# Kernel optimization log

Measured on AMD Instinct MI355X. Metric: run time of the kernel, lower is better.

The kernel has to match this reference:

```python
import jax, jax.numpy as jnp
import numpy as np

B, N_PER, H, EMB, V, S, L = 128, 205, 200, 768, 50265, 512, 6
N = B * N_PER

def conv1d(x, w, b, pad):
    # x: [B, Cin, L], w: [Cout, Cin, K]
    out = jax.lax.conv_general_dilated(x, w, (1,), [(pad, pad)],
                                       dimension_numbers=('NCH', 'OIH', 'NCH'))
    return out + b[None, :, None]

def setup_inputs() -> dict:
    key = jax.random.key(0)
    ks = jax.random.split(key, 24)
    s = lambda fan: 1.0 / np.sqrt(fan)
    inp = {
        'x': jax.random.normal(ks[0], (N, H), jnp.float32),
        'edge_index': jax.random.randint(ks[1], (2, 209920), 0, N, jnp.int32),
        'input_ids': jax.random.randint(ks[2], (B, S), 0, V, jnp.int32),
        'embed_table': jax.random.normal(ks[3], (V, EMB), jnp.float32) * 0.02,
        'ggc_w': jax.random.normal(ks[4], (L, H, H), jnp.float32) * s(H),
        'gru_wih': jax.random.normal(ks[5], (3 * H, H), jnp.float32) * s(H),
        'gru_whh': jax.random.normal(ks[6], (3 * H, H), jnp.float32) * s(H),
        'gru_bih': jnp.zeros((3 * H,), jnp.float32),
        'gru_bhh': jnp.zeros((3 * H,), jnp.float32),
        'conv0_w': jax.random.normal(ks[7], (200, 200, 3), jnp.float32) * s(200 * 3),
        'conv0_b': jnp.zeros((200,), jnp.float32),
        'conv1_w': jax.random.normal(ks[8], (200, EMB, 3), jnp.float32) * s(EMB * 3),
        'conv1_b': jnp.zeros((200,), jnp.float32),
        'conv2_w': jax.random.normal(ks[9], (200, EMB, 4), jnp.float32) * s(EMB * 4),
        'conv2_b': jnp.zeros((200,), jnp.float32),
        'conv3_w': jax.random.normal(ks[10], (200, EMB, 5), jnp.float32) * s(EMB * 5),
        'conv3_b': jnp.zeros((200,), jnp.float32),
        'fc1_w': jax.random.normal(ks[11], (256, 800), jnp.float32) * s(800),
        'fc1_b': jnp.zeros((256,), jnp.float32),
        'fc2_w': jax.random.normal(ks[12], (128, 256), jnp.float32) * s(256),
        'fc2_b': jnp.zeros((128,), jnp.float32),
        'fc3_w': jax.random.normal(ks[13], (2, 128), jnp.float32) * s(128),
        'fc3_b': jnp.zeros((2,), jnp.float32),
    }
    return inp

def gated_graph_conv(x, edge_index, ggc_w, wih, whh, bih, bhh):
    src, dst = edge_index[0], edge_index[1]
    h = x  # [N, H], in_dim == out_channels so no padding needed
    for i in range(L):
        m = h @ ggc_w[i]                                   # [N, H]
        agg = jax.ops.segment_sum(m[src], dst, num_segments=N)  # scatter-add at targets
        gi = agg @ wih.T + bih                             # [N, 3H]
        gh = h @ whh.T + bhh
        ir, iz, inn = jnp.split(gi, 3, axis=1)
        hr, hz, hn = jnp.split(gh, 3, axis=1)
        r = jax.nn.sigmoid(ir + hr)
        z = jax.nn.sigmoid(iz + hz)
        n = jnp.tanh(inn + r * hn)
        h = (1.0 - z) * n + z * h
    return h

def reference(x, edge_index, input_ids, embed_table, ggc_w, gru_wih, gru_whh,
              gru_bih, gru_bhh, conv0_w, conv0_b, conv1_w, conv1_b, conv2_w,
              conv2_b, conv3_w, conv3_b, fc1_w, fc1_b, fc2_w, fc2_b, fc3_w, fc3_b):
    g = gated_graph_conv(x, edge_index, ggc_w, gru_wih, gru_whh, gru_bih, gru_bhh)
    g = g.reshape(B, N_PER, H).transpose(0, 2, 1)          # [B, 200, N_PER]
    e = embed_table[input_ids].transpose(0, 2, 1)          # [B, 768, S]
    x0 = jax.nn.relu(conv1d(g, conv0_w, conv0_b, 1))
    x1 = jax.nn.relu(conv1d(e, conv1_w, conv1_b, 0))
    x2 = jax.nn.relu(conv1d(e, conv2_w, conv2_b, 0))
    x3 = jax.nn.relu(conv1d(e, conv3_w, conv3_b, 0))
    feats = jnp.concatenate([x0.max(axis=2), x1.max(axis=2),
                             x2.max(axis=2), x3.max(axis=2)], axis=1)  # [B, 800]
    h = jax.nn.relu(feats @ fc1_w.T + fc1_b)   # dropout is identity in eval
    h = jax.nn.relu(h @ fc2_w.T + fc2_b)
    return h @ fc3_w.T + fc3_b                 # [B, 2]
```

## Files before the change

kernel.cpp:

```cpp
#include <hip/hip_runtime.h>
#include <math.h>

namespace {

constexpr int NB    = 128;
constexpr int NPER  = 205;
constexpr int H     = 200;
constexpr int EMBD  = 768;
constexpr int SEQ   = 512;
constexpr int NLAY  = 6;
constexpr int NNODE = NB * NPER;
constexpr int NEDGE = 209920;

typedef __bf16 bf16;
typedef _Float16 f16;
typedef __attribute__((ext_vector_type(8))) __bf16 bf16x8;
typedef __attribute__((ext_vector_type(8))) _Float16 f16x8;
typedef __attribute__((ext_vector_type(4))) float f32x4;
typedef unsigned short ushort8 __attribute__((ext_vector_type(8)));
typedef float float4v __attribute__((ext_vector_type(4)));

__device__ __forceinline__ float sigm(float x) { return 1.0f / (1.0f + expf(-x)); }

__device__ __forceinline__ unsigned short f2bf(float x) {
    unsigned int u = __float_as_uint(x);
    unsigned int r = (u + 0x7fffu + ((u >> 16) & 1u)) >> 16;
    return (unsigned short)r;
}
__device__ __forceinline__ unsigned short f2h(float x) {
    union { f16 h; unsigned short u; } c;
    c.h = (f16)x;
    return c.u;
}
__device__ __forceinline__ float h2f(unsigned short u) {
    union { unsigned short u; f16 h; } c;
    c.u = u;
    return (float)c.h;
}

__device__ __forceinline__ int pk_unit(int row, int s) {
    int q = row >> 1;
    return q * 8 + ((((row & 1) << 2) | s) ^ (q & 7));
}

template<bool BIAS, bool OUTF16>
__global__ __launch_bounds__(256, 4)
void gemm_w64(const unsigned short* __restrict__ A, int lda,
              const unsigned short* __restrict__ B,
              const float* __restrict__ bias, int Mreal, int Nreal,
              float* __restrict__ Cf, unsigned short* __restrict__ Ch,
              int ldc, int Kpad)
{
    __shared__ unsigned short As[128 * 64];
    __shared__ unsigned short Bs[128 * 64];

    const int p0 = blockIdx.x * 128;
    const int o0 = blockIdx.y * 128;
    const int tid = threadIdx.x, lane = tid & 63, wid = tid >> 6;
    const int wm = wid >> 1, wn = wid & 1;
    const int lrow = lane & 15, lk = lane >> 4;

    f32x4 acc[4][4];
    #pragma unroll
    for (int i = 0; i < 4; ++i)
        #pragma unroll
        for (int j = 0; j < 4; ++j) acc[i][j] = (f32x4){0.f, 0.f, 0.f, 0.f};

    for (int c0 = 0; c0 < Kpad; c0 += 64) {
        __syncthreads();
        for (int i = wid; i < 32; i += 4) {
            if (i < 16) {
                int u = i * 64 + lane;
                int row = u >> 3, slot = u & 7;
                int ss = slot ^ (row & 7);
                const unsigned short* sA = A + (size_t)(p0 + row) * lda + c0 + ss * 8;
                __builtin_amdgcn_global_load_lds(
                    (const __attribute__((address_space(1))) void*)sA,
                    (__attribute__((address_space(3))) void*)(As + i * 512), 16, 0, 0);
            } else {
                int i2 = i - 16;
                int u = i2 * 64 + lane;
                int row = u >> 3, slot = u & 7;
                int ss = slot ^ (row & 7);
                const unsigned short* sB = B + (size_t)(o0 + row) * Kpad + c0 + ss * 8;
                __builtin_amdgcn_global_load_lds(
                    (const __attribute__((address_space(1))) void*)sB,
                    (__attribute__((address_space(3))) void*)(Bs + i2 * 512), 16, 0, 0);
            }
        }
        __syncthreads();
        #pragma unroll
        for (int hf = 0; hf < 2; ++hf) {
            f16x8 vb[4];
            #pragma unroll
            for (int fn = 0; fn < 4; ++fn) {
                int r = wn * 64 + fn * 16 + lrow;
                int sl = (hf * 4 + lk) ^ (r & 7);
                vb[fn] = *reinterpret_cast<const f16x8*>(&Bs[r * 64 + sl * 8]);
            }
            #pragma unroll
            for (int fm = 0; fm < 4; ++fm) {
                int r = wm * 64 + fm * 16 + lrow;
                int sl = (hf * 4 + lk) ^ (r & 7);
                f16x8 va = *reinterpret_cast<const f16x8*>(&As[r * 64 + sl * 8]);
                #pragma unroll
                for (int fn = 0; fn < 4; ++fn)
                    acc[fm][fn] = __builtin_amdgcn_mfma_f32_16x16x32_f16(va, vb[fn], acc[fm][fn], 0, 0, 0);
            }
        }
    }
    #pragma unroll
    for (int fn = 0; fn < 4; ++fn) {
        int o = o0 + wn * 64 + fn * 16 + lrow;
        if (o >= Nreal) continue;
        float bv = BIAS ? bias[o] : 0.0f;
        #pragma unroll
        for (int fm = 0; fm < 4; ++fm) {
            #pragma unroll
            for (int i = 0; i < 4; ++i) {
                int p = p0 + wm * 64 + fm * 16 + lk * 4 + i;
                if (p >= Mreal) continue;
                float v = acc[fm][fn][i] + bv;
                if (OUTF16) Ch[(size_t)p * ldc + o] = f2h(v);
                else        Cf[(size_t)p * ldc + o] = v;
            }
        }
    }
}

__global__ __launch_bounds__(256, 2)
void gemm_gru(const unsigned short* __restrict__ A,
              const unsigned short* __restrict__ B,
              const float* __restrict__ bb,
              unsigned short* __restrict__ Hn)
{
    __shared__ unsigned short As[2][128 * 64];
    __shared__ unsigned short Bs[2][128 * 64];

    const int p0 = blockIdx.x * 128;
    const int o0 = blockIdx.y * 128;
    const int tid = threadIdx.x, lane = tid & 63, wid = tid >> 6;
    const int wm = wid >> 1, wn = wid & 1;
    const int lrow = lane & 15, lk = lane >> 4;

    auto stage = [&](int bs, int c0) {
        for (int i = wid; i < 32; i += 4) {
            if (i < 16) {
                int u = i * 64 + lane;
                int row = u >> 3, slot = u & 7;
                int ss = slot ^ (row & 7);
                const unsigned short* sA = A + (size_t)(p0 + row) * 512 + c0 + ss * 8;
                __builtin_amdgcn_global_load_lds(
                    (const __attribute__((address_space(1))) void*)sA,
                    (__attribute__((address_space(3))) void*)(&As[bs][i * 512]), 16, 0, 0);
            } else {
                int i2 = i - 16;
                int u = i2 * 64 + lane;
                int row = u >> 3, slot = u & 7;
                int ss = slot ^ (row & 7);
                const unsigned short* sB = B + (size_t)(o0 + row) * 512 + c0 + ss * 8;
                __builtin_amdgcn_global_load_lds(
                    (const __attribute__((address_space(1))) void*)sB,
                    (__attribute__((address_space(3))) void*)(&Bs[bs][i2 * 512]), 16, 0, 0);
            }
        }
    };

    f32x4 acc[4][4];
    #pragma unroll
    for (int i = 0; i < 4; ++i)
        #pragma unroll
        for (int j = 0; j < 4; ++j) acc[i][j] = (f32x4){0.f, 0.f, 0.f, 0.f};

    stage(0, 0);
    __syncthreads();
    int bs = 0;
    for (int t = 0; t < 8; ++t) {
        if (t + 1 < 8) stage(bs ^ 1, (t + 1) * 64);
        const unsigned short* Asc = As[bs];
        const unsigned short* Bsc = Bs[bs];
        #pragma unroll
        for (int hf = 0; hf < 2; ++hf) {
            f16x8 vb[4];
            #pragma unroll
            for (int fn = 0; fn < 4; ++fn) {
                int r = wn * 64 + fn * 16 + lrow;
                int sl = (hf * 4 + lk) ^ (r & 7);
                vb[fn] = *reinterpret_cast<const f16x8*>(&Bsc[r * 64 + sl * 8]);
            }
            #pragma unroll
            for (int fm = 0; fm < 4; ++fm) {
                int r = wm * 64 + fm * 16 + lrow;
                int sl = (hf * 4 + lk) ^ (r & 7);
                f16x8 va = *reinterpret_cast<const f16x8*>(&Asc[r * 64 + sl * 8]);
                #pragma unroll
                for (int fn = 0; fn < 4; ++fn)
                    acc[fm][fn] = __builtin_amdgcn_mfma_f32_16x16x32_f16(va, vb[fn], acc[fm][fn], 0, 0, 0);
            }
        }
        __syncthreads();
        bs ^= 1;
    }

    const int colbase = o0 + wn * 64;
    const int c = (colbase >> 2) + lrow;
    float b0 = bb[colbase + 0 * 16 + lrow];
    float b1 = bb[colbase + 1 * 16 + lrow];
    float b2 = bb[colbase + 2 * 16 + lrow];
    float b3 = bb[colbase + 3 * 16 + lrow];
    #pragma unroll
    for (int fm = 0; fm < 4; ++fm) {
        #pragma unroll
        for (int i = 0; i < 4; ++i) {
            int p = p0 + wm * 64 + fm * 16 + lk * 4 + i;
            size_t hidx = (size_t)p * 512 + 256 + c;
            if (c < H) {
                float r = sigm(acc[fm][0][i] + b0);
                float z = sigm(acc[fm][1][i] + b1);
                float nn = tanhf((acc[fm][2][i] + b2) + r * (acc[fm][3][i] + b3));
                float ho = h2f(A[hidx]);
                Hn[hidx] = f2h((1.0f - z) * nn + z * ho);
            } else {
                Hn[hidx] = 0;
            }
        }
    }
}

template<int K, int CINP, int LIN, int LOUT>
__global__ __launch_bounds__(512, 4)
void conv_w64(const unsigned short* __restrict__ E, const unsigned short* __restrict__ WT,
              const float* __restrict__ bias, int COUT,
              float* __restrict__ feats, int foff)
{
    constexpr int AROWS  = 272;
    constexpr int AINSTR = AROWS * 4 / 64;
    constexpr int BINSTR = K * 128 * 4 / 64;
    __shared__ unsigned short As[AROWS * 32];
    __shared__ unsigned short Bs[K * 128 * 32];

    const int p0 = blockIdx.x * 256;
    const int o0 = blockIdx.y * 128;
    const int b  = blockIdx.z;
    const int tid = threadIdx.x, lane = tid & 63, wid = tid >> 6;
    const int wm = wid >> 1, wn = wid & 1;
    const int lrow = lane & 15, lk = lane >> 4;

    const unsigned short* Eb = E + (size_t)b * LIN * CINP;

    f32x4 acc[4][4];
    #pragma unroll
    for (int i = 0; i < 4; ++i)
        #pragma unroll
        for (int j = 0; j < 4; ++j) acc[i][j] = (f32x4){0.f, 0.f, 0.f, 0.f};

    for (int c0 = 0; c0 < CINP; c0 += 32) {
        __syncthreads();
        for (int i = wid; i < AINSTR + BINSTR; i += 8) {
            if (i < AINSTR) {
                int u = i * 64 + lane;
                int q = u >> 3, cs = u & 7;
                int bsw = cs ^ (q & 7);
                int row = q * 2 + (bsw >> 2), s = bsw & 3;
                int srow = p0 + row; if (srow > LIN - 1) srow = LIN - 1;
                const unsigned short* src = Eb + (size_t)srow * CINP + c0 + s * 8;
                __builtin_amdgcn_global_load_lds(
                    (const __attribute__((address_space(1))) void*)src,
                    (__attribute__((address_space(3))) void*)(As + i * 512), 16, 0, 0);
            } else {
                int i2 = i - AINSTR;
                int u = i2 * 64 + lane;
                int q = u >> 3, cs = u & 7;
                int bsw = cs ^ (q & 7);
                int R = q * 2 + (bsw >> 2), s = bsw & 3;
                int k = R >> 7, r = R & 127;
                const unsigned short* src = WT + ((size_t)k * 256 + o0 + r) * CINP + c0 + s * 8;
                __builtin_amdgcn_global_load_lds(
                    (const __attribute__((address_space(1))) void*)src,
                    (__attribute__((address_space(3))) void*)(Bs + i2 * 512), 16, 0, 0);
            }
        }
        __syncthreads();
        #pragma unroll
        for (int k = 0; k < K; ++k) {
            bf16x8 vb[4];
            #pragma unroll
            for (int fn = 0; fn < 4; ++fn) {
                int R = k * 128 + wn * 64 + fn * 16 + lrow;
                vb[fn] = *reinterpret_cast<const bf16x8*>(&Bs[pk_unit(R, lk) * 8]);
            }
            #pragma unroll
            for (int fm = 0; fm < 4; ++fm) {
                int r = wm * 64 + fm * 16 + lrow + k;
                bf16x8 va = *reinterpret_cast<const bf16x8*>(&As[pk_unit(r, lk) * 8]);
                #pragma unroll
                for (int fn = 0; fn < 4; ++fn)
                    acc[fm][fn] = __builtin_amdgcn_mfma_f32_16x16x32_bf16(va, vb[fn], acc[fm][fn], 0, 0, 0);
            }
        }
    }
    #pragma unroll
    for (int fn = 0; fn < 4; ++fn) {
        int o = o0 + wn * 64 + fn * 16 + lrow;
        float mx = 0.0f;
        if (o < COUT) {
            float bv = bias[o];
            #pragma unroll
            for (int fm = 0; fm < 4; ++fm)
                #pragma unroll
                for (int i = 0; i < 4; ++i) {
                    int p = p0 + wm * 64 + fm * 16 + lk * 4 + i;
                    if (p < LOUT) mx = fmaxf(mx, acc[fm][fn][i] + bv);
                }
        }
        mx = fmaxf(mx, __shfl_xor(mx, 16));
        mx = fmaxf(mx, __shfl_xor(mx, 32));
        if (lane < 16 && o < COUT)
            atomicMax((int*)&feats[(size_t)b * 800 + foff + o], __float_as_int(mx));
    }
}

__global__ void hist_kernel(const int* __restrict__ dst, int* __restrict__ deg)
{
    int e = blockIdx.x * 256 + threadIdx.x;
    if (e < NEDGE) atomicAdd(&deg[dst[e]], 1);
}

__global__ void scan_kernel(const int* __restrict__ deg, int* __restrict__ off, int* __restrict__ cur)
{
    __shared__ int part[1024];
    const int tid = threadIdx.x;
    const int CH = (NNODE + 1023) / 1024;
    int base = tid * CH;
    int s = 0;
    for (int i = 0; i < CH; ++i) { int idx = base + i; s += (idx < NNODE ? deg[idx] : 0); }
    part[tid] = s;
    __syncthreads();
    for (int d = 1; d < 1024; d <<= 1) {
        int v = (tid >= d) ? part[tid - d] : 0;
        __syncthreads();
        part[tid] += v;
        __syncthreads();
    }
    int run = tid ? part[tid - 1] : 0;
    for (int i = 0; i < CH; ++i) {
        int idx = base + i;
        if (idx < NNODE) { off[idx] = run; cur[idx] = run; run += deg[idx]; }
    }
    if (tid == 1023) off[NNODE] = run;
}

__global__ void fill_kernel(const int* __restrict__ src, const int* __restrict__ dst,
                            int* __restrict__ cur, int* __restrict__ eidx)
{
    int e = blockIdx.x * 256 + threadIdx.x;
    if (e >= NEDGE) return;
    int d = dst[e];
    int pos = atomicAdd(&cur[d], 1);
    eidx[pos] = src[e];
}

__global__ void gather_h2(const int* __restrict__ off, const int* __restrict__ eidx,
                          unsigned short* __restrict__ acat)
{
    int t = blockIdx.x * 256 + threadIdx.x;
    if (t >= NNODE * 32) return;
    int c8 = t & 31, n = t >> 5;
    float s[8] = {0.f, 0.f, 0.f, 0.f, 0.f, 0.f, 0.f, 0.f};
    if (c8 < 25) {
        const size_t cb = (size_t)c8 * 8;
        int beg = off[n], end = off[n + 1];
        for (int i = beg; i < end; ++i) {
            int sn = eidx[i];
            ushort8 hh = *(const ushort8*)(acat + (size_t)sn * 512 + 256 + cb);
            #pragma unroll
            for (int j = 0; j < 8; ++j) s[j] += h2f(hh[j]);
        }
    }
    ushort8 o;
    #pragma unroll
    for (int j = 0; j < 8; ++j) o[j] = f2h(s[j]);
    *(ushort8*)(acat + (size_t)n * 512 + c8 * 8) = o;
}

__global__ void h0_kernel(const float* __restrict__ x, unsigned short* __restrict__ acat)
{
    int t = blockIdx.x * 256 + threadIdx.x;
    if (t >= NNODE * 32) return;
    int c8 = t & 31, n = t >> 5;
    ushort8 o = {0,0,0,0,0,0,0,0};
    if (c8 < 25) {
        const float* src = x + (size_t)n * H + c8 * 8;
        float4v v0 = *(const float4v*)src;
        float4v v1 = *(const float4v*)(src + 4);
        o[0] = f2h(v0[0]); o[1] = f2h(v0[1]); o[2] = f2h(v0[2]); o[3] = f2h(v0[3]);
        o[4] = f2h(v1[0]); o[5] = f2h(v1[1]); o[6] = f2h(v1[2]); o[7] = f2h(v1[3]);
    }
    *(ushort8*)(acat + (size_t)n * 512 + 256 + c8 * 8) = o;
}

__global__ void wih16p_prep(const float* __restrict__ wih, unsigned short* __restrict__ w16)
{
    int t = blockIdx.x * 256 + threadIdx.x;
    if (t >= 896 * 32) return;
    int c8 = t & 31, r = t >> 5;
    int g = (r >> 4) & 3;
    int c = (r >> 6) * 16 + (r & 15);
    ushort8 o = {0,0,0,0,0,0,0,0};
    if (g < 3 && c < H) {
        #pragma unroll
        for (int j = 0; j < 8; ++j) {
            int k = c8 * 8 + j;
            if (k < H) o[j] = f2h(wih[(size_t)(g * 200 + c) * H + k]);
        }
    }
    *(ushort8*)(w16 + (size_t)r * 256 + c8 * 8) = o;
}

__global__ void wl_prep(const float* __restrict__ w, unsigned short* __restrict__ wl)
{
    int t = blockIdx.x * 256 + threadIdx.x;
    if (t >= NLAY * 256 * 32) return;
    int c8 = t & 31;
    int rest = t >> 5;
    int jr = rest & 255;
    int l = rest >> 8;
    ushort8 o = {0,0,0,0,0,0,0,0};
    if (jr < H) {
        #pragma unroll
        for (int j = 0; j < 8; ++j) {
            int k = c8 * 8 + j;
            if (k < H) o[j] = f2h(w[(size_t)l * H * H + (size_t)jr * H + k]);
        }
    }
    *(ushort8*)(wl + (size_t)l * 65536 + (size_t)jr * 256 + c8 * 8) = o;
}

__global__ void wf_rightp(const float* __restrict__ whh, const float* __restrict__ bih,
                          const float* __restrict__ bhh,
                          unsigned short* __restrict__ Wf, float* __restrict__ bb)
{
    int t = blockIdx.x * 256 + threadIdx.x;
    if (t >= NLAY * 896 * 32) return;
    int c8 = t & 31;
    int rest = t >> 5;
    int r = rest % 896;
    int l = rest / 896;
    int g = (r >> 4) & 3;
    int c = (r >> 6) * 16 + (r & 15);
    ushort8 o = {0,0,0,0,0,0,0,0};
    if (c < H) {
        #pragma unroll
        for (int j = 0; j < 8; ++j) {
            int kk = c8 * 8 + j;
            float v = 0.0f;
            if (kk < H) {
                if (g == 0)      v = whh[(size_t)c * H + kk];
                else if (g == 1) v = whh[(size_t)(200 + c) * H + kk];
                else if (g == 3) v = whh[(size_t)(400 + c) * H + kk];
            }
            o[j] = f2h(v);
        }
    }
    *(ushort8*)(Wf + (size_t)l * 458752 + (size_t)r * 512 + 256 + c8 * 8) = o;
    if (l == 0 && c8 == 0) {
        float bv = 0.0f;
        if (c < H) {
            if (g == 0)      bv = bih[c] + bhh[c];
            else if (g == 1) bv = bih[200 + c] + bhh[200 + c];
            else if (g == 2) bv = bih[400 + c];
            else             bv = bhh[400 + c];
        }
        bb[r] = bv;
    }
}

__global__ void embed_bf16_kernel(const int* __restrict__ ids, const float* __restrict__ table,
                                  unsigned short* __restrict__ e)
{
    int t = blockIdx.x * 256 + threadIdx.x;
    const int total = NB * SEQ * (EMBD / 8);
    if (t >= total) return;
    int j = t % (EMBD / 8), row = t / (EMBD / 8);
    int id = ids[row];
    const float* src = table + (size_t)id * EMBD + j * 8;
    float4v v0 = *(const float4v*)src;
    float4v v1 = *(const float4v*)(src + 4);
    ushort8 o;
    o[0] = f2bf(v0[0]); o[1] = f2bf(v0[1]); o[2] = f2bf(v0[2]); o[3] = f2bf(v0[3]);
    o[4] = f2bf(v1[0]); o[5] = f2bf(v1[1]); o[6] = f2bf(v1[2]); o[7] = f2bf(v1[3]);
    *(ushort8*)(e + (size_t)row * EMBD + j * 8) = o;
}

__global__ void h_pad_from_acat(const unsigned short* __restrict__ acat,
                                unsigned short* __restrict__ e0)
{
    int t = blockIdx.x * 256 + threadIdx.x;
    const int total = NB * 208 * 32;
    if (t >= total) return;
    int c8 = t % 32, rest = t / 32;
    int r = rest % 208, b = rest / 208;
    ushort8 o = {0,0,0,0,0,0,0,0};
    if (r >= 1 && r <= 205) {
        int node = b * NPER + (r - 1);
        ushort8 hh = *(const ushort8*)(acat + (size_t)node * 512 + 256 + c8 * 8);
        #pragma unroll
        for (int j = 0; j < 8; ++j) o[j] = f2bf(h2f(hh[j]));
    }
    *(ushort8*)(e0 + ((size_t)(b * 208 + r)) * 256 + c8 * 8) = o;
}

__global__ void wconv_bf16_kernel(const float* __restrict__ w, unsigned short* __restrict__ wt,
                                  int K, int CINP, int CINR, int COUT)
{
    long long t = (long long)blockIdx.x * 256 + threadIdx.x;
    long long total = (long long)K * 256 * CINP;
    if (t >= total) return;
    int cin = (int)(t % CINP);
    long long rest = t / CINP;
    int o = (int)(rest % 256), k = (int)(rest / 256);
    float v = 0.0f;
    if (o < COUT && cin < CINR) v = w[((size_t)o * CINR + cin) * K + k];
    wt[t] = f2bf(v);
}

__global__ __launch_bounds__(256)
void fc_head(const float* __restrict__ feats,
             const float* __restrict__ w1, const float* __restrict__ b1,
             const float* __restrict__ w2, const float* __restrict__ b2,
             const float* __restrict__ w3, const float* __restrict__ b3,
             float* __restrict__ out)
{
    __shared__ float f[800];
    __shared__ float h1[256];
    __shared__ float h2[128];
    const int b = blockIdx.x, tid = threadIdx.x;
    for (int i = tid; i < 800; i += 256) f[i] = feats[(size_t)b * 800 + i];
    __syncthreads();
    {
        float acc = b1[tid];
        const float* wr = w1 + (size_t)tid * 800;
        for (int k = 0; k < 800; ++k) acc = fmaf(f[k], wr[k], acc);
        h1[tid] = fmaxf(acc, 0.0f);
    }
    __syncthreads();
    if (tid < 128) {
        float acc = b2[tid];
        const float* wr = w2 + (size_t)tid * 256;
        for (int k = 0; k < 256; ++k) acc = fmaf(h1[k], wr[k], acc);
        h2[tid] = fmaxf(acc, 0.0f);
    }
    __syncthreads();
    if (tid < 2) {
        float acc = b3[tid];
        const float* wr = w3 + (size_t)tid * 128;
        for (int k = 0; k < 128; ++k) acc = fmaf(h2[k], wr[k], acc);
        out[(size_t)b * 2 + tid] = acc;
    }
}

}

extern "C" void kernel_launch(void* const* d_in, const int* in_sizes, int n_in,
                              void* d_out, int out_size, void* d_ws, size_t ws_size,
                              hipStream_t stream)
{
    const float* x         = (const float*)d_in[0];
    const int*   edge      = (const int*)d_in[1];
    const int*   input_ids = (const int*)d_in[2];
    const float* table     = (const float*)d_in[3];
    const float* ggc_w     = (const float*)d_in[4];
    const float* wih       = (const float*)d_in[5];
    const float* whh       = (const float*)d_in[6];
    const float* bih       = (const float*)d_in[7];
    const float* bhh       = (const float*)d_in[8];
    const float* c0w = (const float*)d_in[9];  const float* c0b = (const float*)d_in[10];
    const float* c1w = (const float*)d_in[11]; const float* c1b = (const float*)d_in[12];
    const float* c2w = (const float*)d_in[13]; const float* c2b = (const float*)d_in[14];
    const float* c3w = (const float*)d_in[15]; const float* c3b = (const float*)d_in[16];
    const float* f1w = (const float*)d_in[17]; const float* f1b = (const float*)d_in[18];
    const float* f2w = (const float*)d_in[19]; const float* f2b = (const float*)d_in[20];
    const float* f3w = (const float*)d_in[21]; const float* f3b = (const float*)d_in[22];
    float* out = (float*)d_out;

    float* ws = (float*)d_ws;
    unsigned short* acat_a = (unsigned short*)(ws + 0);
    unsigned short* acat_b = (unsigned short*)(ws + 6717440);
    unsigned short* Wf     = (unsigned short*)(ws + 13434880);
    unsigned short* wl16   = (unsigned short*)(ws + 14811136);
    unsigned short* wih16p = (unsigned short*)(ws + 15007744);
    float* b_big = ws + 15122432;
    int* deg  = (int*)(ws + 15123328);
    int* off  = (int*)(ws + 15149568);
    int* cur  = (int*)(ws + 15175809);
    int* eidx = (int*)(ws + 15202050);
    unsigned short* e_bf16 = (unsigned short*)(ws + 0);
    unsigned short* e0     = (unsigned short*)(ws + 25165824);
    unsigned short* wt0    = (unsigned short*)(ws + 28600000);
    unsigned short* wt1    = wt0 + (size_t)3 * 256 * 256;
    unsigned short* wt2    = wt1 + (size_t)3 * 256 * EMBD;
    unsigned short* wt3    = wt2 + (size_t)4 * 256 * EMBD;
    float* feats = ws + 29900000;

    const int* srcp = edge;
    const int* dstp = edge + NEDGE;

    dim3 blk(256);
    dim3 blk512(512);

    hipMemsetAsync(deg, 0, sizeof(int) * NNODE, stream);
    hipMemsetAsync(acat_b, 0, (size_t)NNODE * 512 * 2, stream);
    hist_kernel<<<dim3((NEDGE + 255) / 256), blk, 0, stream>>>(dstp, deg);
    scan_kernel<<<dim3(1), dim3(1024), 0, stream>>>(deg, off, cur);
    fill_kernel<<<dim3((NEDGE + 255) / 256), blk, 0, stream>>>(srcp, dstp, cur, eidx);
    h0_kernel<<<dim3((NNODE * 32 + 255) / 256), blk, 0, stream>>>(x, acat_a);
    wih16p_prep<<<dim3((896 * 32 + 255) / 256), blk, 0, stream>>>(wih, wih16p);
    wl_prep<<<dim3((NLAY * 256 * 32 + 255) / 256), blk, 0, stream>>>(ggc_w, wl16);
    hipMemsetAsync(Wf, 0, (size_t)NLAY * 896 * 512 * 2, stream);
    wf_rightp<<<dim3((NLAY * 896 * 32 + 255) / 256), blk, 0, stream>>>(whh, bih, bhh, Wf, b_big);
    for (int l = 0; l < NLAY; ++l) {
        gemm_w64<false, true><<<dim3(7, 2), blk, 0, stream>>>(
            wih16p, 256, wl16 + (size_t)l * 65536, nullptr, 896, 200,
            nullptr, Wf + (size_t)l * 458752, 512, 256);
    }

    unsigned short* bufs[2] = { acat_a, acat_b };
    for (int l = 0; l < NLAY; ++l) {
        unsigned short* curb = bufs[l & 1];
        unsigned short* nxtb = bufs[(l + 1) & 1];
        gather_h2<<<dim3((NNODE * 32 + 255) / 256), blk, 0, stream>>>(off, eidx, curb);
        gemm_gru<<<dim3(NNODE / 128, 7), blk, 0, stream>>>(
            curb, Wf + (size_t)l * 458752, b_big, nxtb);
    }

    h_pad_from_acat<<<dim3((NB * 208 * 32 + 255) / 256), blk, 0, stream>>>(acat_a, e0);
    embed_bf16_kernel<<<dim3(NB * SEQ * (EMBD / 8) / 256), blk, 0, stream>>>(input_ids, table, e_bf16);
    wconv_bf16_kernel<<<dim3((3 * 256 * 256 + 255) / 256), blk, 0, stream>>>(c0w, wt0, 3, 256, 200, 200);
    wconv_bf16_kernel<<<dim3((3 * 256 * EMBD + 255) / 256), blk, 0, stream>>>(c1w, wt1, 3, EMBD, EMBD, 200);
    wconv_bf16_kernel<<<dim3((4 * 256 * EMBD + 255) / 256), blk, 0, stream>>>(c2w, wt2, 4, EMBD, EMBD, 200);
    wconv_bf16_kernel<<<dim3((5 * 256 * EMBD + 255) / 256), blk, 0, stream>>>(c3w, wt3, 5, EMBD, EMBD, 200);

    hipMemsetAsync(feats, 0, sizeof(float) * NB * 800, stream);
    conv_w64<3, 256, 208, 205><<<dim3(1, 2, NB), blk512, 0, stream>>>(e0, wt0, c0b, 200, feats, 0);
    conv_w64<3, EMBD, SEQ, 510><<<dim3(2, 2, NB), blk512, 0, stream>>>(e_bf16, wt1, c1b, 200, feats, 200);
    conv_w64<4, EMBD, SEQ, 509><<<dim3(2, 2, NB), blk512, 0, stream>>>(e_bf16, wt2, c2b, 200, feats, 400);
    conv_w64<5, EMBD, SEQ, 508><<<dim3(2, 2, NB), blk512, 0, stream>>>(e_bf16, wt3, c3b, 200, feats, 600);

    fc_head<<<dim3(NB), blk, 0, stream>>>(feats, f1w, f1b, f2w, f2b, f3w, f3b, out);
}
```

Measured before the change: 1.040 ms.

## Shrink concatenated GRU operand row stride from 512 to 448 and batch weight GEMMs

Repacks the concatenated [aggregated | hidden] fp16 operand and fused GRU weight rows from a 512 stride to 448, with the hidden half at offset 224. The GRU GEMM then runs 7 K-iterations instead of 8, which cuts MFMA work and memory traffic per layer. The per-layer weight-fusion GEMMs are merged into one launch using blockIdx.z, and the memset of the second activation buffer is removed, since the padding columns are no longer written. The gather kernel is unrolled by four edges to get more loads in flight. The risk is that stale padding in the alternate buffer must stay harmless: padding columns 200-223 in acat_b are never zeroed, so their contents depend on the matching weight columns being zero.

```diff
diff --git a/kernel.cpp b/kernel.cpp
--- a/kernel.cpp
+++ b/kernel.cpp
@@ -11,6 +11,8 @@
 constexpr int NLAY  = 6;
 constexpr int NNODE = NB * NPER;
 constexpr int NEDGE = 209920;
+constexpr int KP    = 448;
+constexpr int HOFF  = 224;
 
 typedef __bf16 bf16;
 typedef _Float16 f16;
@@ -46,9 +48,9 @@
 template<bool BIAS, bool OUTF16>
 __global__ __launch_bounds__(256, 4)
 void gemm_w64(const unsigned short* __restrict__ A, int lda,
-              const unsigned short* __restrict__ B,
+              const unsigned short* __restrict__ B, size_t strideBz,
               const float* __restrict__ bias, int Mreal, int Nreal,
-              float* __restrict__ Cf, unsigned short* __restrict__ Ch,
+              float* __restrict__ Cf, unsigned short* __restrict__ Ch, size_t strideCz,
               int ldc, int Kpad)
 {
     __shared__ unsigned short As[128 * 64];
@@ -56,6 +58,7 @@
 
     const int p0 = blockIdx.x * 128;
     const int o0 = blockIdx.y * 128;
+    const unsigned short* Bz = B + (size_t)blockIdx.z * strideBz;
     const int tid = threadIdx.x, lane = tid & 63, wid = tid >> 6;
     const int wm = wid >> 1, wn = wid & 1;
     const int lrow = lane & 15, lk = lane >> 4;
@@ -82,7 +85,7 @@
                 int u = i2 * 64 + lane;
                 int row = u >> 3, slot = u & 7;
                 int ss = slot ^ (row & 7);
-                const unsigned short* sB = B + (size_t)(o0 + row) * Kpad + c0 + ss * 8;
+                const unsigned short* sB = Bz + (size_t)(o0 + row) * Kpad + c0 + ss * 8;
                 __builtin_amdgcn_global_load_lds(
                     (const __attribute__((address_space(1))) void*)sB,
                     (__attribute__((address_space(3))) void*)(Bs + i2 * 512), 16, 0, 0);
@@ -121,8 +124,8 @@
                 int p = p0 + wm * 64 + fm * 16 + lk * 4 + i;
                 if (p >= Mreal) continue;
                 float v = acc[fm][fn][i] + bv;
-                if (OUTF16) Ch[(size_t)p * ldc + o] = f2h(v);
-                else        Cf[(size_t)p * ldc + o] = v;
+                if (OUTF16) Ch[(size_t)blockIdx.z * strideCz + (size_t)p * ldc + o] = f2h(v);
+                else        Cf[(size_t)blockIdx.z * strideCz + (size_t)p * ldc + o] = v;
             }
         }
     }
@@ -149,7 +152,7 @@
                 int u = i * 64 + lane;
                 int row = u >> 3, slot = u & 7;
                 int ss = slot ^ (row & 7);
-                const unsigned short* sA = A + (size_t)(p0 + row) * 512 + c0 + ss * 8;
+                const unsigned short* sA = A + (size_t)(p0 + row) * KP + c0 + ss * 8;
                 __builtin_amdgcn_global_load_lds(
                     (const __attribute__((address_space(1))) void*)sA,
                     (__attribute__((address_space(3))) void*)(&As[bs][i * 512]), 16, 0, 0);
@@ -158,7 +161,7 @@
                 int u = i2 * 64 + lane;
                 int row = u >> 3, slot = u & 7;
                 int ss = slot ^ (row & 7);
-                const unsigned short* sB = B + (size_t)(o0 + row) * 512 + c0 + ss * 8;
+                const unsigned short* sB = B + (size_t)(o0 + row) * KP + c0 + ss * 8;
                 __builtin_amdgcn_global_load_lds(
                     (const __attribute__((address_space(1))) void*)sB,
                     (__attribute__((address_space(3))) void*)(&Bs[bs][i2 * 512]), 16, 0, 0);
@@ -175,8 +178,9 @@
     stage(0, 0);
     __syncthreads();
     int bs = 0;
-    for (int t = 0; t < 8; ++t) {
-        if (t + 1 < 8) stage(bs ^ 1, (t + 1) * 64);
+    constexpr int NIT = KP / 64;
+    for (int t = 0; t < NIT; ++t) {
+        if (t + 1 < NIT) stage(bs ^ 1, (t + 1) * 64);
         const unsigned short* Asc = As[bs];
         const unsigned short* Bsc = Bs[bs];
         #pragma unroll
@@ -213,15 +217,13 @@
         #pragma unroll
         for (int i = 0; i < 4; ++i) {
             int p = p0 + wm * 64 + fm * 16 + lk * 4 + i;
-            size_t hidx = (size_t)p * 512 + 256 + c;
             if (c < H) {
+                size_t hidx = (size_t)p * KP + HOFF + c;
                 float r = sigm(acc[fm][0][i] + b0);
                 float z = sigm(acc[fm][1][i] + b1);
                 float nn = tanhf((acc[fm][2][i] + b2) + r * (acc[fm][3][i] + b3));
                 float ho = h2f(A[hidx]);
                 Hn[hidx] = f2h((1.0f - z) * nn + z * ho);
-            } else {
-                Hn[hidx] = 0;
             }
         }
     }
@@ -366,21 +368,31 @@
     int t = blockIdx.x * 256 + threadIdx.x;
     if (t >= NNODE * 32) return;
     int c8 = t & 31, n = t >> 5;
+    if (c8 >= 25) return;
+    const size_t cb = (size_t)c8 * 8;
     float s[8] = {0.f, 0.f, 0.f, 0.f, 0.f, 0.f, 0.f, 0.f};
-    if (c8 < 25) {
-        const size_t cb = (size_t)c8 * 8;
-        int beg = off[n], end = off[n + 1];
-        for (int i = beg; i < end; ++i) {
-            int sn = eidx[i];
-            ushort8 hh = *(const ushort8*)(acat + (size_t)sn * 512 + 256 + cb);
-            #pragma unroll
-            for (int j = 0; j < 8; ++j) s[j] += h2f(hh[j]);
-        }
+    int beg = off[n], end = off[n + 1];
+    int i = beg;
+    for (; i + 4 <= end; i += 4) {
+        int s0 = eidx[i], s1 = eidx[i + 1], s2 = eidx[i + 2], s3 = eidx[i + 3];
+        ushort8 a = *(const ushort8*)(acat + (size_t)s0 * KP + HOFF + cb);
+        ushort8 b = *(const ushort8*)(acat + (size_t)s1 * KP + HOFF + cb);
+        ushort8 c = *(const ushort8*)(acat + (size_t)s2 * KP + HOFF + cb);
+        ushort8 d = *(const ushort8*)(acat + (size_t)s3 * KP + HOFF + cb);
+        #pragma unroll
+        for (int j = 0; j < 8; ++j)
+            s[j] += (h2f(a[j]) + h2f(b[j])) + (h2f(c[j]) + h2f(d[j]));
+    }
+    for (; i < end; ++i) {
+        int sn = eidx[i];
+        ushort8 hh = *(const ushort8*)(acat + (size_t)sn * KP + HOFF + cb);
+        #pragma unroll
+        for (int j = 0; j < 8; ++j) s[j] += h2f(hh[j]);
     }
     ushort8 o;
     #pragma unroll
     for (int j = 0; j < 8; ++j) o[j] = f2h(s[j]);
-    *(ushort8*)(acat + (size_t)n * 512 + c8 * 8) = o;
+    *(ushort8*)(acat + (size_t)n * KP + cb) = o;
 }
 
 __global__ void h0_kernel(const float* __restrict__ x, unsigned short* __restrict__ acat)
@@ -388,6 +400,7 @@
     int t = blockIdx.x * 256 + threadIdx.x;
     if (t >= NNODE * 32) return;
     int c8 = t & 31, n = t >> 5;
+    if (c8 >= 28) return;
     ushort8 o = {0,0,0,0,0,0,0,0};
     if (c8 < 25) {
         const float* src = x + (size_t)n * H + c8 * 8;
@@ -396,7 +409,7 @@
         o[0] = f2h(v0[0]); o[1] = f2h(v0[1]); o[2] = f2h(v0[2]); o[3] = f2h(v0[3]);
         o[4] = f2h(v1[0]); o[5] = f2h(v1[1]); o[6] = f2h(v1[2]); o[7] = f2h(v1[3]);
     }
-    *(ushort8*)(acat + (size_t)n * 512 + 256 + c8 * 8) = o;
+    *(ushort8*)(acat + (size_t)n * KP + HOFF + c8 * 8) = o;
 }
 
 __global__ void wih16p_prep(const float* __restrict__ wih, unsigned short* __restrict__ w16)
@@ -441,9 +454,9 @@
                           unsigned short* __restrict__ Wf, float* __restrict__ bb)
 {
     int t = blockIdx.x * 256 + threadIdx.x;
-    if (t >= NLAY * 896 * 32) return;
-    int c8 = t & 31;
-    int rest = t >> 5;
+    if (t >= NLAY * 896 * 28) return;
+    int c8 = t % 28;
+    int rest = t / 28;
     int r = rest % 896;
     int l = rest / 896;
     int g = (r >> 4) & 3;
@@ -462,7 +475,7 @@
             o[j] = f2h(v);
         }
     }
-    *(ushort8*)(Wf + (size_t)l * 458752 + (size_t)r * 512 + 256 + c8 * 8) = o;
+    *(ushort8*)(Wf + (size_t)l * (896 * KP) + (size_t)r * KP + HOFF + c8 * 8) = o;
     if (l == 0 && c8 == 0) {
         float bv = 0.0f;
         if (c < H) {
@@ -501,9 +514,9 @@
     int c8 = t % 32, rest = t / 32;
     int r = rest % 208, b = rest / 208;
     ushort8 o = {0,0,0,0,0,0,0,0};
-    if (r >= 1 && r <= 205) {
+    if (r >= 1 && r <= 205 && c8 < 25) {
         int node = b * NPER + (r - 1);
-        ushort8 hh = *(const ushort8*)(acat + (size_t)node * 512 + 256 + c8 * 8);
+        ushort8 hh = *(const ushort8*)(acat + (size_t)node * KP + HOFF + c8 * 8);
         #pragma unroll
         for (int j = 0; j < 8; ++j) o[j] = f2bf(h2f(hh[j]));
     }
@@ -585,15 +598,15 @@
 
     float* ws = (float*)d_ws;
     unsigned short* acat_a = (unsigned short*)(ws + 0);
-    unsigned short* acat_b = (unsigned short*)(ws + 6717440);
-    unsigned short* Wf     = (unsigned short*)(ws + 13434880);
-    unsigned short* wl16   = (unsigned short*)(ws + 14811136);
-    unsigned short* wih16p = (unsigned short*)(ws + 15007744);
-    float* b_big = ws + 15122432;
-    int* deg  = (int*)(ws + 15123328);
-    int* off  = (int*)(ws + 15149568);
-    int* cur  = (int*)(ws + 15175809);
-    int* eidx = (int*)(ws + 15202050);
+    unsigned short* acat_b = (unsigned short*)(ws + 5877760);
+    unsigned short* Wf     = (unsigned short*)(ws + 11755520);
+    unsigned short* wl16   = (unsigned short*)(ws + 12959744);
+    unsigned short* wih16p = (unsigned short*)(ws + 13156352);
+    float* b_big = ws + 13271040;
+    int* deg  = (int*)(ws + 13271936);
+    int* off  = (int*)(ws + 13298176);
+    int* cur  = (int*)(ws + 13324417);
+    int* eidx = (int*)(ws + 13350658);
     unsigned short* e_bf16 = (unsigned short*)(ws + 0);
     unsigned short* e0     = (unsigned short*)(ws + 25165824);
     unsigned short* wt0    = (unsigned short*)(ws + 28600000);
@@ -609,20 +622,17 @@
     dim3 blk512(512);
 
     hipMemsetAsync(deg, 0, sizeof(int) * NNODE, stream);
-    hipMemsetAsync(acat_b, 0, (size_t)NNODE * 512 * 2, stream);
     hist_kernel<<<dim3((NEDGE + 255) / 256), blk, 0, stream>>>(dstp, deg);
     scan_kernel<<<dim3(1), dim3(1024), 0, stream>>>(deg, off, cur);
     fill_kernel<<<dim3((NEDGE + 255) / 256), blk, 0, stream>>>(srcp, dstp, cur, eidx);
     h0_kernel<<<dim3((NNODE * 32 + 255) / 256), blk, 0, stream>>>(x, acat_a);
     wih16p_prep<<<dim3((896 * 32 + 255) / 256), blk, 0, stream>>>(wih, wih16p);
     wl_prep<<<dim3((NLAY * 256 * 32 + 255) / 256), blk, 0, stream>>>(ggc_w, wl16);
-    hipMemsetAsync(Wf, 0, (size_t)NLAY * 896 * 512 * 2, stream);
-    wf_rightp<<<dim3((NLAY * 896 * 32 + 255) / 256), blk, 0, stream>>>(whh, bih, bhh, Wf, b_big);
-    for (int l = 0; l < NLAY; ++l) {
-        gemm_w64<false, true><<<dim3(7, 2), blk, 0, stream>>>(
-            wih16p, 256, wl16 + (size_t)l * 65536, nullptr, 896, 200,
-            nullptr, Wf + (size_t)l * 458752, 512, 256);
-    }
+    hipMemsetAsync(Wf, 0, (size_t)NLAY * 896 * KP * 2, stream);
+    wf_rightp<<<dim3((NLAY * 896 * 28 + 255) / 256), blk, 0, stream>>>(whh, bih, bhh, Wf, b_big);
+    gemm_w64<false, true><<<dim3(7, 2, NLAY), blk, 0, stream>>>(
+        wih16p, 256, wl16, (size_t)256 * 256, nullptr, 896, 200,
+        nullptr, Wf, (size_t)896 * KP, KP, 256);
 
     unsigned short* bufs[2] = { acat_a, acat_b };
     for (int l = 0; l < NLAY; ++l) {
@@ -630,7 +640,7 @@
         unsigned short* nxtb = bufs[(l + 1) & 1];
         gather_h2<<<dim3((NNODE * 32 + 255) / 256), blk, 0, stream>>>(off, eidx, curb);
         gemm_gru<<<dim3(NNODE / 128, 7), blk, 0, stream>>>(
-            curb, Wf + (size_t)l * 458752, b_big, nxtb);
+            curb, Wf + (size_t)l * (896 * KP), b_big, nxtb);
     }
 
     h_pad_from_acat<<<dim3((NB * 208 * 32 + 255) / 256), blk, 0, stream>>>(acat_a, e0);
```

Result: faster. 905.1 us, median of 3 (-13.0%).
